# Performance work log

Measured on AMD Instinct MI355X. Metric: run time of the kernel, lower is better.

The kernel has to match this reference:

```python
import jax, jax.numpy as jnp
import numpy as np

SDR_SIZE = 2048
CAPACITY = 131072
N_ACTIVE = 40
CONTENT_DIM = 384
THRESHOLD = 0.3
N_PLANTED = 64  # rows made similar to the query so top-k hits pass the threshold


def setup_inputs() -> dict:
    key = jax.random.key(0)
    k1, k2, k3, k4 = jax.random.split(key, 4)
    p = N_ACTIVE / SDR_SIZE
    query_sdr = (jax.random.uniform(k1, (SDR_SIZE,)) < p).astype(jnp.float32)
    sdr_bank = (jax.random.uniform(k2, (CAPACITY, SDR_SIZE)) < p).astype(jnp.float32)
    # plant near-duplicates of the query so retrieval has matches above threshold
    noise = (jax.random.uniform(k4, (N_PLANTED, SDR_SIZE)) < 0.1).astype(jnp.float32)
    planted = jnp.clip(query_sdr[None, :] * (1.0 - noise) + noise * sdr_bank[:N_PLANTED], 0.0, 1.0)
    sdr_bank = sdr_bank.at[:N_PLANTED].set(planted)
    content_bank = jax.random.normal(k3, (CAPACITY, CONTENT_DIM), dtype=jnp.float32)
    valid_mask = jnp.ones((CAPACITY,), dtype=bool)  # buffer is full (count == capacity)
    return {
        "query_sdr": query_sdr,
        "sdr_bank": sdr_bank,
        "content_bank": content_bank,
        "valid_mask": valid_mask,
        "top_k": 32,
    }


def reference(query_sdr, sdr_bank, content_bank, valid_mask, top_k):
    # overlap = number of shared active bits  -> [capacity]
    overlap = sdr_bank @ query_sdr
    similarity = overlap / N_ACTIVE
    similarity = jnp.where(valid_mask, similarity, -jnp.inf)
    top_sim, top_idx = jax.lax.top_k(similarity, top_k)
    # torch version filters by boolean mask (dynamic shape); here we keep
    # fixed shape [top_k] and zero out entries below threshold instead.
    keep = top_sim >= THRESHOLD
    contents = content_bank[top_idx]                      # [top_k, content_dim]
    contents = jnp.where(keep[:, None], contents, 0.0)
    top_sim = jnp.where(keep, top_sim, 0.0)
    return contents, top_sim
```

## Files before the change

### kernel.cpp

```cpp
#include <hip/hip_runtime.h>
#include <stdint.h>

#define SDR_SIZE   2048
#define CAPACITY   131072
#define TOPK       32
#define CDIM       384


__global__ void k_prep(const float* __restrict__ q, int* __restrict__ w) {
    __shared__ int s_cnt;
    __shared__ int s_act[256];
    if (threadIdx.x == 0) s_cnt = 0;
    __syncthreads();
    for (int j = threadIdx.x; j < SDR_SIZE; j += 256) {
        if (q[j] != 0.0f) {
            int p = atomicAdd(&s_cnt, 1);
            if (p < 256) s_act[p] = j;
        }
    }
    __syncthreads();
    if (threadIdx.x == 0) {
        int n = s_cnt < 128 ? s_cnt : 128;
        for (int i = 1; i < n; i++) {
            int v = s_act[i]; int k = i - 1;
            while (k >= 0 && s_act[k] > v) { s_act[k + 1] = s_act[k]; k--; }
            s_act[k + 1] = v;
        }
        w[0] = n;
        w[192] = 0;
        for (int i = 0; i < n; i++) w[4 + i] = s_act[i];
    }
}

__global__ __launch_bounds__(256) void k_overlap(const float* __restrict__ bank,
                                                 const int* __restrict__ mask,
                                                 int* __restrict__ w, int cap) {
    int wave = (int)((blockIdx.x * blockDim.x + threadIdx.x) >> 6);
    int lane = threadIdx.x & 63;
    if (wave >= CAPACITY) return;
    int n_act = w[0];
    const float* rp = bank + (size_t)wave * SDR_SIZE;
    int ov = 0;
    for (int base = 0; base < n_act; base += 64) {
        int l = base + lane;
        float v = 0.0f;
        if (l < n_act) {
            int c = w[4 + l];
            v = rp[c];
        }
        unsigned long long b = __ballot(l < n_act && v != 0.0f);
        ov += __popcll(b);
    }
    if (lane == 0) {
        float sim = (float)ov / 40.0f;
        if (mask[wave] != 0 && sim >= 0.3f) {
            int p = atomicAdd(&w[192], 1);
            if (p < cap) w[256 + p] = (ov << 17) | (131071 - wave);
        }
    }
}

__global__ void k_select(const float* __restrict__ content,
                         const int* __restrict__ w,
                         float* __restrict__ out, int cap) {
    __shared__ unsigned int s_top[TOPK];
    __shared__ unsigned int s_red[256];
    int t = threadIdx.x;
    int m = w[192];
    if (m > cap) m = cap;
    int kcount = (m < TOPK) ? m : TOPK;
    unsigned int prev = 0xFFFFFFFFu;
    for (int s = 0; s < kcount; s++) {
        unsigned int best = 0;
        for (int i = t; i < m; i += 256) {
            unsigned int k = (unsigned int)w[256 + i];
            if (k < prev && k > best) best = k;
        }
        __syncthreads();
        s_red[t] = best;
        __syncthreads();
        for (int off = 128; off > 0; off >>= 1) {
            if (t < off) s_red[t] = s_red[t] > s_red[t + off] ? s_red[t] : s_red[t + off];
            __syncthreads();
        }
        prev = s_red[0];
        if (t == 0) s_top[s] = prev;
    }
    __syncthreads();
    for (int i = t; i < TOPK * CDIM; i += 256) {
        int s = i / CDIM, d = i - s * CDIM;
        float val = 0.0f;
        if (s < kcount) {
            int idx = CAPACITY - 1 - (int)(s_top[s] & 0x1FFFFu);
            val = content[(size_t)idx * CDIM + d];
        }
        out[i] = val;
    }
    if (t < TOPK) {
        float sv = 0.0f;
        if (t < kcount) sv = (float)(s_top[t] >> 17) / 40.0f;
        out[TOPK * CDIM + t] = sv;
    }
}

extern "C" void kernel_launch(void* const* d_in, const int* in_sizes, int n_in,
                              void* d_out, int out_size, void* d_ws, size_t ws_size,
                              hipStream_t stream) {
    const float* query   = (const float*)d_in[0];
    const float* bank    = (const float*)d_in[1];
    const float* content = (const float*)d_in[2];
    const int* mask      = (const int*)d_in[3];
    float* out = (float*)d_out;
    int* w = (int*)d_ws;

    size_t words = ws_size / 4;
    int cap = (int)((words > 256) ? (words - 256) : 0);
    if (cap > 65536) cap = 65536;

    k_prep<<<1, 256, 0, stream>>>(query, w);
    k_overlap<<<CAPACITY / 4, 256, 0, stream>>>(bank, mask, w, cap);
    k_select<<<1, 256, 0, stream>>>(content, w, out, cap);
}
```

Baseline: 1.360 ms.

## Assign eight bank rows per wave and use shuffle reductions in selection

The overlap kernel now gives each wave eight rows instead of one. Each 8-lane group gathers that row's active columns and reduces its count with xor-shuffles. This cuts the grid eightfold and keeps more lanes busy, since only about 40 active bits exist per query. The selection kernel runs its iterative top-k with a single wave using shuffle max-reductions, which removes shared-memory tree reductions and block-wide barriers. Gathers now fan out across eight rows per wave, so the memory access pattern is more scattered.

```diff
diff --git a/kernel.cpp b/kernel.cpp
--- a/kernel.cpp
+++ b/kernel.cpp
@@ -5,6 +5,7 @@
 #define CAPACITY   131072
 #define TOPK       32
 #define CDIM       384
+#define RPW        8
 
 
 __global__ void k_prep(const float* __restrict__ q, int* __restrict__ w) {
@@ -35,27 +36,25 @@
 __global__ __launch_bounds__(256) void k_overlap(const float* __restrict__ bank,
                                                  const int* __restrict__ mask,
                                                  int* __restrict__ w, int cap) {
-    int wave = (int)((blockIdx.x * blockDim.x + threadIdx.x) >> 6);
-    int lane = threadIdx.x & 63;
-    if (wave >= CAPACITY) return;
-    int n_act = w[0];
-    const float* rp = bank + (size_t)wave * SDR_SIZE;
+    const int wave = (blockIdx.x * 256 + (int)threadIdx.x) >> 6;
+    const int lane = threadIdx.x & 63;
+    const int sub  = lane & 7;
+    const int row  = wave * RPW + (lane >> 3);
+    const int nact = w[0];
+    const float* rp = bank + (size_t)row * SDR_SIZE;
     int ov = 0;
-    for (int base = 0; base < n_act; base += 64) {
-        int l = base + lane;
-        float v = 0.0f;
-        if (l < n_act) {
-            int c = w[4 + l];
-            v = rp[c];
-        }
-        unsigned long long b = __ballot(l < n_act && v != 0.0f);
-        ov += __popcll(b);
+    for (int idx = sub; idx < nact; idx += 8) {
+        int c = w[4 + idx];
+        ov += (rp[c] != 0.0f) ? 1 : 0;
     }
-    if (lane == 0) {
+    ov += __shfl_xor(ov, 1);
+    ov += __shfl_xor(ov, 2);
+    ov += __shfl_xor(ov, 4);
+    if (sub == 0) {
         float sim = (float)ov / 40.0f;
-        if (mask[wave] != 0 && sim >= 0.3f) {
+        if (mask[row] != 0 && sim >= 0.3f) {
             int p = atomicAdd(&w[192], 1);
-            if (p < cap) w[256 + p] = (ov << 17) | (131071 - wave);
+            if (p < cap) w[256 + p] = (ov << 17) | (131071 - row);
         }
     }
 }
@@ -64,27 +63,25 @@
                          const int* __restrict__ w,
                          float* __restrict__ out, int cap) {
     __shared__ unsigned int s_top[TOPK];
-    __shared__ unsigned int s_red[256];
     int t = threadIdx.x;
     int m = w[192];
     if (m > cap) m = cap;
     int kcount = (m < TOPK) ? m : TOPK;
-    unsigned int prev = 0xFFFFFFFFu;
-    for (int s = 0; s < kcount; s++) {
-        unsigned int best = 0;
-        for (int i = t; i < m; i += 256) {
-            unsigned int k = (unsigned int)w[256 + i];
-            if (k < prev && k > best) best = k;
+    if (t < 64) {
+        unsigned int prev = 0xFFFFFFFFu;
+        for (int s = 0; s < kcount; s++) {
+            unsigned int best = 0;
+            for (int i = t; i < m; i += 64) {
+                unsigned int k = (unsigned int)w[256 + i];
+                if (k < prev && k > best) best = k;
+            }
+            for (int off = 1; off < 64; off <<= 1) {
+                unsigned int o = (unsigned int)__shfl_xor((int)best, off);
+                best = o > best ? o : best;
+            }
+            prev = best;
+            if (t == 0) s_top[s] = best;
         }
-        __syncthreads();
-        s_red[t] = best;
-        __syncthreads();
-        for (int off = 128; off > 0; off >>= 1) {
-            if (t < off) s_red[t] = s_red[t] > s_red[t + off] ? s_red[t] : s_red[t + off];
-            __syncthreads();
-        }
-        prev = s_red[0];
-        if (t == 0) s_top[s] = prev;
     }
     __syncthreads();
     for (int i = t; i < TOPK * CDIM; i += 256) {
@@ -118,6 +115,6 @@
     if (cap > 65536) cap = 65536;
 
     k_prep<<<1, 256, 0, stream>>>(query, w);
-    k_overlap<<<CAPACITY / 4, 256, 0, stream>>>(bank, mask, w, cap);
+    k_overlap<<<CAPACITY / (RPW * 4), 256, 0, stream>>>(bank, mask, w, cap);
     k_select<<<1, 256, 0, stream>>>(content, w, out, cap);
 }
```

Result: no change. 1.357 ms (-0.2%).
